# Performance work log

Hardware: AMD Instinct MI355X
Metric: run time of the kernel (lower is better)

The kernel has to match this reference:

```python
import jax, jax.numpy as jnp
import numpy as np

HEADS = 8
NUM_CLASS = 4
DIM = 512


def setup_inputs() -> dict:
    key = jax.random.key(0)
    k0, k1, k2, k3 = jax.random.split(key, 4)
    B, N, C = 4, 1280, DIM  # N = (NUM_CLASS+1) * 256 tokens per group
    x = jax.random.normal(k0, (B, N, C), jnp.float32)
    # modality-presence mask: 1 = modality available, 0 = missing
    mask = jax.random.randint(k1, (B, NUM_CLASS), 0, 2).astype(jnp.int32)
    s = 1.0 / np.sqrt(C)
    W_qkv = jax.random.normal(k2, (C, 3 * C), jnp.float32) * s  # qkv (no bias)
    W_proj = jax.random.normal(k3, (C, C), jnp.float32) * s
    b_proj = jnp.zeros((C,), jnp.float32)
    return {"x": x, "mask": mask, "W_qkv": W_qkv, "W_proj": W_proj, "b_proj": b_proj}


def reference(x, mask, W_qkv, W_proj, b_proj):
    B, N, C = x.shape
    H = HEADS
    hd = C // H
    scale = hd ** -0.5
    # qkv: [B,N,3C] -> [3,B,H,N,hd]
    qkv = (x @ W_qkv).reshape(B, N, 3, H, hd).transpose(2, 0, 3, 1, 4)
    q, k, v = qkv[0], qkv[1], qkv[2]
    attn = jnp.einsum('bhqd,bhkd->bhqk', q, k) * scale  # [B,H,N,N]
    # block mask: keys belonging to missing modality groups are disallowed;
    # the last (fusion) group is always allowed -> every row has valid keys.
    np_ = N // (NUM_CLASS + 1)  # tokens per group
    group = jnp.arange(N) // np_  # [N], group id in [0, NUM_CLASS]
    allowed = jnp.concatenate(
        [mask.astype(jnp.float32), jnp.ones((B, 1), jnp.float32)], axis=1)  # [B, NUM_CLASS+1]
    col_ok = allowed[:, group]  # [B, N] per-key allowance
    attn = jnp.where(col_ok[:, None, None, :] == 0, -jnp.inf, attn)
    attn = jax.nn.softmax(attn, axis=-1)
    out = jnp.einsum('bhqk,bhkd->bhqd', attn, v)  # [B,H,N,hd]
    out = out.transpose(0, 2, 1, 3).reshape(B, N, C)
    out = out @ W_proj + b_proj
    return out, attn
```

## Files before the change

kernel.cpp:

```cpp
#include <hip/hip_runtime.h>
#include <math.h>

#define BATCH 4
#define NSEQ  1280
#define CDIM  512
#define HEADS 8
#define HD    64
#define NT    20
#define NQT   20

typedef __attribute__((ext_vector_type(8))) short bf16x8;
typedef __attribute__((ext_vector_type(4))) float f32x4;

#define MFMA16(a,b,c) __builtin_amdgcn_mfma_f32_16x16x32_bf16(a,b,c,0,0,0)

__device__ __forceinline__ unsigned short f2bf(float f) {
    union { float f; unsigned int u; } v; v.f = f;
    unsigned int r = v.u + 0x7fffu + ((v.u >> 16) & 1u);
    return (unsigned short)(r >> 16);
}
__device__ __forceinline__ float bf2f(unsigned short h) {
    union { unsigned int u; float f; } v; v.u = ((unsigned int)h) << 16;
    return v.f;
}
__device__ __forceinline__ void gload_lds16(const void* g, void* l) {
    __builtin_amdgcn_global_load_lds(
        (const __attribute__((address_space(1))) unsigned int*)g,
        (__attribute__((address_space(3))) unsigned int*)l, 16, 0, 0);
}

__global__ __launch_bounds__(256)
void conv_kernel(const float* __restrict__ x, const float* __restrict__ Wq,
                 const float* __restrict__ Wp, unsigned short* __restrict__ xb,
                 unsigned short* __restrict__ Wqt, unsigned short* __restrict__ Wpt)
{
    __shared__ float lt[64][65];
    const int bx = blockIdx.x;
    const int tid = threadIdx.x;
    if (bx < 1280) {
        const int u = bx * 256 + tid;
        const int m = u >> 6;
        const int b6 = u & 63;
        const int chunk = b6 >> 3;
        const int blk = b6 & 7;
        const float* src = x + (size_t)m * 512 + b6 * 8;
        bf16x8 hv;
        #pragma unroll
        for (int j = 0; j < 8; ++j) hv[j] = (short)f2bf(src[j]);
        *(bf16x8*)(xb + (size_t)m * 512 + chunk * 64 + ((blk ^ (m & 7)) * 8)) = hv;
    } else {
        int wi = bx - 1280;
        const float* W; unsigned short* Wt; int N, kt, nt; bool isQ;
        if (wi < 192) { W = Wq; Wt = Wqt; N = 1536; kt = wi / 24; nt = wi % 24; isQ = true; }
        else { wi -= 192; W = Wp; Wt = Wpt; N = 512; kt = wi / 8; nt = wi % 8; isQ = false; }
        const int k0 = kt * 64, n0 = nt * 64;
        {
            const int r = tid >> 4;
            const int c = (tid & 15) * 4;
            #pragma unroll
            for (int i = 0; i < 4; ++i) {
                const float4 v = *(const float4*)(W + (size_t)(k0 + r + i * 16) * N + n0 + c);
                lt[r + i * 16][c + 0] = v.x; lt[r + i * 16][c + 1] = v.y;
                lt[r + i * 16][c + 2] = v.z; lt[r + i * 16][c + 3] = v.w;
            }
        }
        __syncthreads();
        #pragma unroll
        for (int i = 0; i < 2; ++i) {
            const int u = tid + i * 256;
            const int n = u >> 3;
            const int blk = u & 7;
            const int kin = (blk ^ (n & 7)) * 8;
            const float sc = (isQ && (n0 + n) < 512) ? 0.125f : 1.0f;
            bf16x8 o;
            #pragma unroll
            for (int j = 0; j < 8; ++j) o[j] = (short)f2bf(lt[kin + j][n] * sc);
            *(bf16x8*)(Wt + (size_t)(n0 + n) * 512 + k0 + blk * 8) = o;
        }
    }
}

template<int WM, int WN, bool BIAS, bool OUTBF16>
__global__ __launch_bounds__(256)
void gemm_bf16(const unsigned short* __restrict__ A,
               const unsigned short* __restrict__ B,
               const float* __restrict__ bias, void* __restrict__ Cv,
               int M, int N, int KA)
{
    constexpr int BM = 2 * WM, BN = 2 * WN;
    constexpr int MI = WM / 16, NI = WN / 16;
    __shared__ __align__(16) unsigned short smem[(BM + BN) * 64];
    unsigned short* As = smem;
    unsigned short* Bs = smem + BM * 64;

    const int tid = threadIdx.x;
    const int w = tid >> 6, lane = tid & 63;
    const int l15 = lane & 15, hi = lane >> 4;
    const int wr = w >> 1, wc = w & 1;

    const int nb = gridDim.x;
    const int L = (blockIdx.x & 7) * (nb >> 3) + (blockIdx.x >> 3);
    const int nx = N / BN;
    const int m0 = (L / nx) * BM, n0 = (L % nx) * BN;

    f32x4 acc[MI][NI];
    #pragma unroll
    for (int mi = 0; mi < MI; ++mi)
        #pragma unroll
        for (int ni = 0; ni < NI; ++ni) acc[mi][ni] = (f32x4){0.f, 0.f, 0.f, 0.f};

    constexpr int LA = BM * 128 / 4096;
    constexpr int LB = BN * 128 / 4096;

    for (int k0 = 0; k0 < KA; k0 += 64) {
        #pragma unroll
        for (int i = 0; i < LA; ++i) {
            const int off = tid * 16 + i * 4096;
            const int row = off >> 7, cb = off & 127;
            gload_lds16((const char*)A + ((size_t)(m0 + row) * KA + k0) * 2 + cb,
                        (char*)As + off);
        }
        #pragma unroll
        for (int i = 0; i < LB; ++i) {
            const int off = tid * 16 + i * 4096;
            const int row = off >> 7, cb = off & 127;
            gload_lds16((const char*)B + ((size_t)(n0 + row) * 512 + k0) * 2 + cb,
                        (char*)Bs + off);
        }
        __syncthreads();
        #pragma unroll
        for (int kk = 0; kk < 2; ++kk) {
            bf16x8 af[MI], bfr[NI];
            #pragma unroll
            for (int mi = 0; mi < MI; ++mi) {
                const int row = wr * WM + mi * 16 + l15;
                af[mi] = *(const bf16x8*)(As + row * 64 + ((kk * 4 + hi) ^ (row & 7)) * 8);
            }
            #pragma unroll
            for (int ni = 0; ni < NI; ++ni) {
                const int row = wc * WN + ni * 16 + l15;
                bfr[ni] = *(const bf16x8*)(Bs + row * 64 + ((kk * 4 + hi) ^ (row & 7)) * 8);
            }
            #pragma unroll
            for (int mi = 0; mi < MI; ++mi)
                #pragma unroll
                for (int ni = 0; ni < NI; ++ni)
                    acc[mi][ni] = MFMA16(af[mi], bfr[ni], acc[mi][ni]);
        }
        __syncthreads();
    }

    if (OUTBF16) {
        unsigned short* C = (unsigned short*)Cv;
        #pragma unroll
        for (int mi = 0; mi < MI; ++mi)
            #pragma unroll
            for (int ni = 0; ni < NI; ++ni)
                #pragma unroll
                for (int r = 0; r < 4; ++r)
                    smem[(wr * WM + mi * 16 + hi * 4 + r) * BN + wc * WN + ni * 16 + l15] =
                        f2bf(acc[mi][ni][r]);
        __syncthreads();
        constexpr int UNITS = BM * BN / 8 / 256;
        #pragma unroll
        for (int i = 0; i < UNITS; ++i) {
            const int u = tid + i * 256;
            const int row = u / (BN / 8), cb = u % (BN / 8);
            *(bf16x8*)(C + (size_t)(m0 + row) * N + n0 + cb * 8) =
                *(const bf16x8*)(smem + row * BN + cb * 8);
        }
    } else {
        float* C = (float*)Cv;
        #pragma unroll
        for (int mi = 0; mi < MI; ++mi)
            #pragma unroll
            for (int ni = 0; ni < NI; ++ni) {
                const int col = n0 + wc * WN + ni * 16 + l15;
                const float bv = BIAS ? bias[col] : 0.f;
                #pragma unroll
                for (int r = 0; r < 4; ++r)
                    C[(size_t)(m0 + wr * WM + mi * 16 + hi * 4 + r) * N + col] =
                        acc[mi][ni][r] + bv;
            }
    }
}

__global__ __launch_bounds__(256)
void vprep_kernel(const unsigned short* __restrict__ qkvb,
                  unsigned short* __restrict__ Vt)
{
    __shared__ __align__(16) unsigned short vt[64][72];
    const int bx = blockIdx.x;
    const int ntile = bx % NQT;
    const int bh = bx / NQT;
    const int b = bh >> 3, h = bh & 7;
    const int n0 = ntile * 64;
    const int tid = threadIdx.x;
    const unsigned short* base = qkvb + (size_t)(b * NSEQ + n0) * 1536 + 1024 + h * HD;

    #pragma unroll
    for (int i = 0; i < 2; ++i) {
        const int u = tid + i * 256;
        const int n = u >> 3;
        const int dg = u & 7;
        *(bf16x8*)&vt[n][dg * 8] = *(const bf16x8*)(base + (size_t)n * 1536 + dg * 8);
    }
    __syncthreads();
    #pragma unroll
    for (int i = 0; i < 2; ++i) {
        const int u = tid + i * 256;
        const int d = u >> 3;
        const int kb = u & 7;
        const int kin = (kb ^ (d & 7)) * 8;
        bf16x8 o;
        #pragma unroll
        for (int j = 0; j < 8; ++j) o[j] = (short)vt[kin + j][d];
        *(bf16x8*)(Vt + ((size_t)(bh * HD + d)) * NSEQ + n0 + kb * 8) = o;
    }
}

__global__ __launch_bounds__(256)
void attn_mfma(const unsigned short* __restrict__ qkvb,
               const unsigned short* __restrict__ Vt,
               const int* __restrict__ mask,
               float* __restrict__ attn, unsigned short* __restrict__ outh)
{
    __shared__ __align__(16) unsigned short kbuf[2][4096];
    __shared__ __align__(16) unsigned short vbuf[2][4096];
    __shared__ float ps[64][68];

    const int bx = blockIdx.x;
    const int bh = bx & 31;
    const int qt = bx >> 5;
    const int b = bh >> 3, h = bh & 7;
    const int tid = threadIdx.x;
    const int w = tid >> 6;
    const int lane = tid & 63;
    const int l15 = lane & 15;
    const int hi = lane >> 4;
    const int q0 = qt * 64;

    unsigned int amask = 0xF0000u;
    #pragma unroll
    for (int g = 0; g < 4; ++g)
        if (mask[b * 4 + g] != 0) amask |= (0xFu << (g * 4));

    const unsigned short* qrow =
        qkvb + (size_t)(b * NSEQ + q0 + w * 16 + l15) * 1536 + h * HD;
    const bf16x8 aq0 = *(const bf16x8*)(qrow + hi * 8);
    const bf16x8 aq1 = *(const bf16x8*)(qrow + 32 + hi * 8);

    const unsigned short* ks = qkvb + (size_t)b * NSEQ * 1536 + 512 + h * HD;
    const unsigned short* vg = Vt + (size_t)bh * HD * NSEQ;

    #define STAGE_K(t, buf)                                                      \
        { _Pragma("unroll")                                                      \
          for (int half_ = 0; half_ < 2; ++half_) {                              \
            const int idx_ = half_ * 256 + tid;                                  \
            const int row_ = idx_ >> 3, blk_ = idx_ & 7;                         \
            gload_lds16(ks + (size_t)((t) * 64 + row_) * 1536                    \
                           + ((blk_ ^ (row_ & 7)) * 8),                          \
                        (char*)&(buf)[0] + idx_ * 16); } }
    #define STAGE_V(t, buf)                                                      \
        { _Pragma("unroll")                                                      \
          for (int half_ = 0; half_ < 2; ++half_) {                              \
            const int idx_ = half_ * 256 + tid;                                  \
            const int row_ = idx_ >> 3, blk_ = idx_ & 7;                         \
            gload_lds16(vg + (size_t)row_ * NSEQ + (t) * 64 + blk_ * 8,          \
                        (char*)&(buf)[0] + idx_ * 16); } }

    float lr[4] = {0.f, 0.f, 0.f, 0.f};

    int t0 = 0;
    while (!((amask >> t0) & 1u)) ++t0;

    STAGE_K(t0, kbuf[0]);
    __syncthreads();
    int cur = 0, t = t0;
    while (t < NT) {
        int tn = t + 1;
        while (tn < NT && !((amask >> tn) & 1u)) ++tn;
        if (tn < NT) STAGE_K(tn, kbuf[cur ^ 1]);
        f32x4 accS[4];
        #pragma unroll
        for (int cb = 0; cb < 4; ++cb) accS[cb] = (f32x4){0.f, 0.f, 0.f, 0.f};
        #pragma unroll
        for (int cb = 0; cb < 4; ++cb) {
            const int row = cb * 16 + l15;
            const char* bp = (const char*)&kbuf[cur][0] + row * 128;
            const bf16x8 b0 = *(const bf16x8*)(bp + ((hi ^ (row & 7)) * 16));
            const bf16x8 b1 = *(const bf16x8*)(bp + (((4 + hi) ^ (row & 7)) * 16));
            accS[cb] = MFMA16(aq0, b0, accS[cb]);
            accS[cb] = MFMA16(aq1, b1, accS[cb]);
        }
        #pragma unroll
        for (int cb = 0; cb < 4; ++cb)
            #pragma unroll
            for (int r = 0; r < 4; ++r)
                lr[r] += __expf(accS[cb][r]);
        __syncthreads();
        cur ^= 1; t = tn;
    }

    float rl[4];
    #pragma unroll
    for (int r = 0; r < 4; ++r) {
        float s = lr[r];
        s += __shfl_xor(s, 1);
        s += __shfl_xor(s, 2);
        s += __shfl_xor(s, 4);
        s += __shfl_xor(s, 8);
        rl[r] = 1.f / s;
    }

    {
        float* arow = attn + ((size_t)bh * NSEQ + q0 + w * 16) * NSEQ;
        const float4 z = make_float4(0.f, 0.f, 0.f, 0.f);
        for (int tz = 0; tz < NT; ++tz) {
            if ((amask >> tz) & 1u) continue;
            #pragma unroll
            for (int rr = 0; rr < 4; ++rr)
                *(float4*)(arow + (size_t)(rr * 4 + hi) * NSEQ + tz * 64 + l15 * 4) = z;
        }
    }

    STAGE_K(t0, kbuf[0]);
    STAGE_V(t0, vbuf[0]);
    __syncthreads();
    f32x4 accO[4];
    #pragma unroll
    for (int db = 0; db < 4; ++db) accO[db] = (f32x4){0.f, 0.f, 0.f, 0.f};

    cur = 0; t = t0;
    while (t < NT) {
        int tn = t + 1;
        while (tn < NT && !((amask >> tn) & 1u)) ++tn;
        if (tn < NT) {
            STAGE_K(tn, kbuf[cur ^ 1]);
            STAGE_V(tn, vbuf[cur ^ 1]);
        }
        f32x4 accS[4];
        #pragma unroll
        for (int cb = 0; cb < 4; ++cb) accS[cb] = (f32x4){0.f, 0.f, 0.f, 0.f};
        #pragma unroll
        for (int cb = 0; cb < 4; ++cb) {
            const int row = cb * 16 + l15;
            const char* bp = (const char*)&kbuf[cur][0] + row * 128;
            const bf16x8 b0 = *(const bf16x8*)(bp + ((hi ^ (row & 7)) * 16));
            const bf16x8 b1 = *(const bf16x8*)(bp + (((4 + hi) ^ (row & 7)) * 16));
            accS[cb] = MFMA16(aq0, b0, accS[cb]);
            accS[cb] = MFMA16(aq1, b1, accS[cb]);
        }
        #pragma unroll
        for (int cb = 0; cb < 4; ++cb)
            #pragma unroll
            for (int r = 0; r < 4; ++r)
                ps[w * 16 + hi * 4 + r][cb * 16 + l15] =
                    __expf(accS[cb][r]) * rl[r];

        {
            float* arow = attn + ((size_t)bh * NSEQ + q0 + w * 16) * NSEQ + t * 64;
            #pragma unroll
            for (int rr = 0; rr < 4; ++rr) {
                const float4 pv = *(const float4*)&ps[w * 16 + rr * 4 + hi][l15 * 4];
                *(float4*)(arow + (size_t)(rr * 4 + hi) * NSEQ + l15 * 4) = pv;
            }
        }

        #pragma unroll
        for (int s = 0; s < 2; ++s) {
            const float4 p0 = *(const float4*)&ps[w * 16 + l15][s * 32 + hi * 8];
            const float4 p1 = *(const float4*)&ps[w * 16 + l15][s * 32 + hi * 8 + 4];
            bf16x8 pa;
            pa[0] = (short)f2bf(p0.x); pa[1] = (short)f2bf(p0.y);
            pa[2] = (short)f2bf(p0.z); pa[3] = (short)f2bf(p0.w);
            pa[4] = (short)f2bf(p1.x); pa[5] = (short)f2bf(p1.y);
            pa[6] = (short)f2bf(p1.z); pa[7] = (short)f2bf(p1.w);
            #pragma unroll
            for (int db = 0; db < 4; ++db) {
                const int row = db * 16 + l15;
                const char* bp = (const char*)&vbuf[cur][0] + row * 128;
                const bf16x8 bv = *(const bf16x8*)(bp + (((4 * s + hi) ^ (row & 7)) * 16));
                accO[db] = MFMA16(pa, bv, accO[db]);
            }
        }
        __syncthreads();
        cur ^= 1; t = tn;
    }

    #pragma unroll
    for (int db = 0; db < 4; ++db)
        #pragma unroll
        for (int r = 0; r < 4; ++r)
            ps[w * 16 + hi * 4 + r][db * 16 + l15] = accO[db][r];
    #pragma unroll
    for (int i = 0; i < 2; ++i) {
        const int u = lane + i * 64;
        const int rowL = u >> 3;
        const int blk = u & 7;
        const float4 p0 = *(const float4*)&ps[w * 16 + rowL][blk * 8];
        const float4 p1 = *(const float4*)&ps[w * 16 + rowL][blk * 8 + 4];
        bf16x8 o;
        o[0] = (short)f2bf(p0.x); o[1] = (short)f2bf(p0.y);
        o[2] = (short)f2bf(p0.z); o[3] = (short)f2bf(p0.w);
        o[4] = (short)f2bf(p1.x); o[5] = (short)f2bf(p1.y);
        o[6] = (short)f2bf(p1.z); o[7] = (short)f2bf(p1.w);
        const int n = q0 + w * 16 + rowL;
        *(bf16x8*)(outh + ((size_t)(b * NSEQ + n)) * 512 + h * 64 + ((blk ^ (n & 7)) * 8)) = o;
    }
    #undef STAGE_K
    #undef STAGE_V
}

extern "C" void kernel_launch(void* const* d_in, const int* in_sizes, int n_in,
                              void* d_out, int out_size, void* d_ws, size_t ws_size,
                              hipStream_t stream)
{
    const float* x      = (const float*)d_in[0];
    const int*   mask   = (const int*)  d_in[1];
    const float* W_qkv  = (const float*)d_in[2];
    const float* W_proj = (const float*)d_in[3];
    const float* b_proj = (const float*)d_in[4];

    float* out  = (float*)d_out;
    float* attn = out + (size_t)BATCH * NSEQ * CDIM;

    char* ws = (char*)d_ws;
    unsigned short* qkvb = (unsigned short*)ws;
    unsigned short* Vt   = (unsigned short*)(ws + 15728640);
    unsigned short* xb   = (unsigned short*)(ws + 15728640 + 5242880);
    unsigned short* Wqt  = xb + (size_t)5120 * 512;
    unsigned short* Wpt  = Wqt + (size_t)1536 * 512;
    unsigned short* outh = Wpt + (size_t)512 * 512;

    const int M = BATCH * NSEQ;

    conv_kernel<<<1536, 256, 0, stream>>>(x, W_qkv, W_proj, xb, Wqt, Wpt);

    gemm_bf16<64, 64, false, true><<<480, 256, 0, stream>>>(
        xb, Wqt, nullptr, qkvb, M, 1536, 512);

    vprep_kernel<<<BATCH * HEADS * NQT, 256, 0, stream>>>(qkvb, Vt);

    attn_mfma<<<BATCH * HEADS * NQT, 256, 0, stream>>>(qkvb, Vt, mask, attn, outh);

    gemm_bf16<32, 64, true, false><<<320, 256, 0, stream>>>(
        outh, Wpt, b_proj, out, M, 512, 512);
}
```

Measured before the change: 91.71 us.

## Compute V transposed directly via swapped GEMM, drop vprep transpose kernel

```diff
diff --git a/kernel.cpp b/kernel.cpp
--- a/kernel.cpp
+++ b/kernel.cpp
@@ -186,42 +186,8 @@
 }
 
 __global__ __launch_bounds__(256)
-void vprep_kernel(const unsigned short* __restrict__ qkvb,
-                  unsigned short* __restrict__ Vt)
-{
-    __shared__ __align__(16) unsigned short vt[64][72];
-    const int bx = blockIdx.x;
-    const int ntile = bx % NQT;
-    const int bh = bx / NQT;
-    const int b = bh >> 3, h = bh & 7;
-    const int n0 = ntile * 64;
-    const int tid = threadIdx.x;
-    const unsigned short* base = qkvb + (size_t)(b * NSEQ + n0) * 1536 + 1024 + h * HD;
-
-    #pragma unroll
-    for (int i = 0; i < 2; ++i) {
-        const int u = tid + i * 256;
-        const int n = u >> 3;
-        const int dg = u & 7;
-        *(bf16x8*)&vt[n][dg * 8] = *(const bf16x8*)(base + (size_t)n * 1536 + dg * 8);
-    }
-    __syncthreads();
-    #pragma unroll
-    for (int i = 0; i < 2; ++i) {
-        const int u = tid + i * 256;
-        const int d = u >> 3;
-        const int kb = u & 7;
-        const int kin = (kb ^ (d & 7)) * 8;
-        bf16x8 o;
-        #pragma unroll
-        for (int j = 0; j < 8; ++j) o[j] = (short)vt[kin + j][d];
-        *(bf16x8*)(Vt + ((size_t)(bh * HD + d)) * NSEQ + n0 + kb * 8) = o;
-    }
-}
-
-__global__ __launch_bounds__(256)
-void attn_mfma(const unsigned short* __restrict__ qkvb,
-               const unsigned short* __restrict__ Vt,
+void attn_mfma(const unsigned short* __restrict__ qkb,
+               const unsigned short* __restrict__ Vtf,
                const int* __restrict__ mask,
                float* __restrict__ attn, unsigned short* __restrict__ outh)
 {
@@ -246,19 +212,19 @@
         if (mask[b * 4 + g] != 0) amask |= (0xFu << (g * 4));
 
     const unsigned short* qrow =
-        qkvb + (size_t)(b * NSEQ + q0 + w * 16 + l15) * 1536 + h * HD;
+        qkb + (size_t)(b * NSEQ + q0 + w * 16 + l15) * 1024 + h * HD;
     const bf16x8 aq0 = *(const bf16x8*)(qrow + hi * 8);
     const bf16x8 aq1 = *(const bf16x8*)(qrow + 32 + hi * 8);
 
-    const unsigned short* ks = qkvb + (size_t)b * NSEQ * 1536 + 512 + h * HD;
-    const unsigned short* vg = Vt + (size_t)bh * HD * NSEQ;
+    const unsigned short* ks = qkb + (size_t)b * NSEQ * 1024 + 512 + h * HD;
+    const unsigned short* vg = Vtf + (size_t)h * HD * 5120 + b * NSEQ;
 
     #define STAGE_K(t, buf)                                                      \
         { _Pragma("unroll")                                                      \
           for (int half_ = 0; half_ < 2; ++half_) {                              \
             const int idx_ = half_ * 256 + tid;                                  \
             const int row_ = idx_ >> 3, blk_ = idx_ & 7;                         \
-            gload_lds16(ks + (size_t)((t) * 64 + row_) * 1536                    \
+            gload_lds16(ks + (size_t)((t) * 64 + row_) * 1024                    \
                            + ((blk_ ^ (row_ & 7)) * 8),                          \
                         (char*)&(buf)[0] + idx_ * 16); } }
     #define STAGE_V(t, buf)                                                      \
@@ -266,7 +232,8 @@
           for (int half_ = 0; half_ < 2; ++half_) {                              \
             const int idx_ = half_ * 256 + tid;                                  \
             const int row_ = idx_ >> 3, blk_ = idx_ & 7;                         \
-            gload_lds16(vg + (size_t)row_ * NSEQ + (t) * 64 + blk_ * 8,          \
+            gload_lds16(vg + (size_t)row_ * 5120 + (t) * 64                      \
+                           + ((blk_ ^ (row_ & 7)) * 8),                          \
                         (char*)&(buf)[0] + idx_ * 16); } }
 
     float lr[4] = {0.f, 0.f, 0.f, 0.f};
@@ -426,9 +393,9 @@
     float* attn = out + (size_t)BATCH * NSEQ * CDIM;
 
     char* ws = (char*)d_ws;
-    unsigned short* qkvb = (unsigned short*)ws;
-    unsigned short* Vt   = (unsigned short*)(ws + 15728640);
-    unsigned short* xb   = (unsigned short*)(ws + 15728640 + 5242880);
+    unsigned short* qkb  = (unsigned short*)ws;
+    unsigned short* Vtf  = qkb + (size_t)5120 * 1024;
+    unsigned short* xb   = Vtf + (size_t)512 * 5120;
     unsigned short* Wqt  = xb + (size_t)5120 * 512;
     unsigned short* Wpt  = Wqt + (size_t)1536 * 512;
     unsigned short* outh = Wpt + (size_t)512 * 512;
@@ -437,12 +404,13 @@
 
     conv_kernel<<<1536, 256, 0, stream>>>(x, W_qkv, W_proj, xb, Wqt, Wpt);
 
-    gemm_bf16<64, 64, false, true><<<480, 256, 0, stream>>>(
-        xb, Wqt, nullptr, qkvb, M, 1536, 512);
-
-    vprep_kernel<<<BATCH * HEADS * NQT, 256, 0, stream>>>(qkvb, Vt);
-
-    attn_mfma<<<BATCH * HEADS * NQT, 256, 0, stream>>>(qkvb, Vt, mask, attn, outh);
+    gemm_bf16<64, 64, false, true><<<320, 256, 0, stream>>>(
+        xb, Wqt, nullptr, qkb, M, 1024, 512);
+
+    gemm_bf16<64, 64, false, true><<<160, 256, 0, stream>>>(
+        Wqt + (size_t)1024 * 512, xb, nullptr, Vtf, 512, 5120, 512);
+
+    attn_mfma<<<BATCH * HEADS * NQT, 256, 0, stream>>>(qkb, Vtf, mask, attn, outh);
 
     gemm_bf16<32, 64, true, false><<<320, 256, 0, stream>>>(
         outh, Wpt, b_proj, out, M, 512, 512);
```

Measured after the change: 98.34 us. +7.2%, slower.
